# Kernel optimization log

Hardware: AMD Instinct MI355X
Metric: run time of the kernel (lower is better)

Reference implementation:

```python
import jax, jax.numpy as jnp
import numpy as np

B, T, C = 4, 1024, 512      # batch, seq_len, n_attn
H, TT, D = 1, 1024, 16      # n_head (forced to 1 by kv.view), ctx_len, head_size


def setup_inputs() -> dict:
    key = jax.random.key(0)
    ks = jax.random.split(key, 13)
    s = 0.02
    return {
        "x": jax.random.normal(ks[0], (B, T, C), jnp.float32),
        "time_w": 1.0 + 0.1 * jax.random.normal(ks[1], (H, TT), jnp.float32),
        "time_alpha": 1.0 + 0.1 * jax.random.normal(ks[2], (H, 1, TT), jnp.float32),
        "time_beta": 1.0 + 0.1 * jax.random.normal(ks[3], (H, TT, 1), jnp.float32),
        "time_gamma": 1.0 + 0.1 * jax.random.normal(ks[4], (TT, 1), jnp.float32),
        "Wk": s * jax.random.normal(ks[5], (D, C), jnp.float32),
        "bk": jnp.zeros((D,), jnp.float32),
        "Wv": s * jax.random.normal(ks[6], (D, C), jnp.float32),
        "bv": jnp.zeros((D,), jnp.float32),
        "Wr": s * jax.random.normal(ks[7], (D, C), jnp.float32),
        "br": jnp.zeros((D,), jnp.float32),
        "Wo": s * jax.random.normal(ks[8], (64, D), jnp.float32),
        "bo": jnp.zeros((64,), jnp.float32),
    }


def reference(x, time_w, time_alpha, time_beta, time_gamma,
              Wk, bk, Wv, bv, Wr, br, Wo, bo):
    Tq = x.shape[1]
    # --- Toeplitz decay-matrix build (pad / tile / reshape trick) ---
    w = jnp.pad(time_w, ((0, 0), (0, TT)))                    # [H, 2TT]
    w = jnp.tile(w, (1, TT))[:, :-TT]                         # [H, 2TT*TT - TT]
    w = w.reshape(-1, TT, 2 * TT - 1)[:, :, TT - 1:]          # [H, TT, TT]
    w = w[:, :Tq, :Tq] * time_alpha[:, :, :Tq] * time_beta[:, :Tq, :]  # [H, T, T]
    # --- time shift on first half of channels (ZeroPad2d((0,0,1,-1))) ---
    half = x.shape[-1] // 2
    xs = jnp.pad(x[:, :, :half], ((0, 0), (1, 0), (0, 0)))[:, :-1]   # shift right by 1
    xx = jnp.concatenate([xs, x[:, :, half:]], axis=-1)              # [B, T, C]
    # --- k / v / r projections ---
    k = jnp.exp(jnp.clip(xx @ Wk.T + bk, -60.0, 30.0))        # [B, T, D]
    v = xx @ Wv.T + bv                                        # [B, T, D]
    r = xx @ Wr.T + br                                        # [B, T, D]
    sum_k = jnp.cumsum(k, axis=1)                             # [B, T, D]
    kv = k * v                                                # [B, T, D]
    # torch: kv.view(B,T,1,D).transpose(1,2) -> [B,1,T,D]; einsum 'htu,bthd->bhud'
    # broadcasts w's h=1 against kv's time axis and kv's t=1 against w's t axis:
    #   wkv[b,h,u,d] = (sum_t w[0,t,u]) * kv[b,h(time),d]
    w_sum = jnp.sum(w, axis=1)[0]                             # [T] over u
    wkv_full = w_sum[None, None, :, None] * kv[:, :, None, :] # [B, T, T, D]
    wkv = jnp.mean(wkv_full, axis=1)                          # mean over h -> [B, T, D]
    rwkv = r * wkv / (sum_k + 1e-8)                           # [B, T, D]
    out = (rwkv @ Wo.T + bo) * time_gamma[:Tq, :]             # [B, T, 64]
    return out
```

## Files before the change

kernel.cpp:

```cpp
#include <hip/hip_runtime.h>
#include <hip/hip_bf16.h>

typedef __hip_bfloat16 bf16;


__device__ __forceinline__ float ldf(const void* p, int f, long idx) {
    if (f == 0) return ((const float*)p)[idx];
    if (f == 1) {
        unsigned int u = ((unsigned int)((const unsigned short*)p)[idx]) << 16;
        float r; __builtin_memcpy(&r, &u, 4); return r;
    }
    return 0.f;
}

__device__ __forceinline__ int sniff_one(const unsigned short* u, int els) {
    int n16 = els < 64 ? els : 64;
    bool allzero = true;
    for (int j = 0; j < n16; ++j) if (u[j] != 0) { allzero = false; break; }
    if (allzero) return 2;
    int npair = n16 / 2;
    for (int j = 0; j < npair; ++j) {
        unsigned short lo = u[2 * j], hi = u[2 * j + 1];
        int elo = (lo >> 7) & 0xFF, ehi = (hi >> 7) & 0xFF;
        bool lo_ok = (elo >= 64 && elo <= 190) || lo == 0;
        bool hi_ok = (ehi >= 64 && ehi <= 190) || hi == 0;
        if (!(lo_ok && hi_ok)) return 0;
    }
    return 1;
}

__global__ __launch_bounds__(256) void setup_kernel(
    const void* x, const void* tw, const void* alpha, const void* beta,
    const void* gamma, const void* Wk, const void* bk, const void* Wv,
    const void* bv, const void* Wr, const void* br, const void* Wo,
    const void* bo,
    int n0, int n1, int n2, int n3, int n4, int n5, int n6, int n7,
    int n8, int n9, int n10, int n11, int n12,
    int* __restrict__ flags,
    float* __restrict__ WT4, float* __restrict__ biasWS,
    float* __restrict__ WoF, float* __restrict__ boF,
    float* __restrict__ gammaF, float* __restrict__ w_sum)
{
    __shared__ int sf[16];
    __shared__ float red[256];
    int tid = threadIdx.x;
    const void* ps[13] = {x,tw,alpha,beta,gamma,Wk,bk,Wv,bv,Wr,br,Wo,bo};
    int ns[13] = {n0,n1,n2,n3,n4,n5,n6,n7,n8,n9,n10,n11,n12};
    if (tid < 13) sf[tid] = sniff_one((const unsigned short*)ps[tid], ns[tid]);
    __syncthreads();
    if (tid == 0) {
        int any16 = 0;
        for (int j = 0; j < 13; ++j) if (sf[j] == 1) any16 = 1;
        sf[13] = any16;
    }
    __syncthreads();
    if (blockIdx.x == 0 && tid < 14) flags[tid] = sf[tid];

    int idx = blockIdx.x * 256 + tid;
    if (idx < 32768) {
        int q = idx >> 8, rem = idx & 255;
        int o = rem >> 2, c = q * 4 + (rem & 3);
        float val = 0.f;
        if (o < 16)      val = ldf(Wk, sf[5], (long)o * 512 + c);
        else if (o < 32) val = ldf(Wv, sf[7], (long)(o - 16) * 512 + c);
        else if (o < 48) val = ldf(Wr, sf[9], (long)(o - 32) * 512 + c);
        WT4[idx] = val;
    } else if (idx < 33792) {
        int i = idx - 32768;
        WoF[i] = ldf(Wo, sf[11], i);
    } else if (idx < 34816) {
        int i = idx - 33792;
        gammaF[i] = ldf(gamma, sf[4], i);
    } else if (idx < 34880) {
        int i = idx - 34816;
        boF[i] = ldf(bo, sf[12], i);
    } else if (idx < 34944) {
        int i = idx - 34880;
        float bb = 0.f;
        if (i < 16)      bb = ldf(bk, sf[6], i);
        else if (i < 32) bb = ldf(bv, sf[8], i - 16);
        else if (i < 48) bb = ldf(br, sf[10], i - 32);
        biasWS[i] = bb;
    }

    int u = blockIdx.x;
    int ftw = sf[1], fal = sf[2], fbe = sf[3];
    float acc = 0.f;
    int n = 1024 - u;
    for (int s = tid; s < n; s += 256)
        acc += ldf(tw, ftw, 1023 - s) * ldf(beta, fbe, u + s);
    red[tid] = acc;
    __syncthreads();
    for (int off = 128; off > 0; off >>= 1) {
        if (tid < off) red[tid] += red[tid + off];
        __syncthreads();
    }
    if (tid == 0) w_sum[u] = red[0] * ldf(alpha, fal, u);
}

__global__ __launch_bounds__(256) void proj_kernel(
    const void* __restrict__ x, const float* __restrict__ WT4,
    const float* __restrict__ biasWS, const int* __restrict__ flg,
    float* __restrict__ k_ws, float* __restrict__ v_ws, float* __restrict__ r_ws)
{
    __shared__ float xs[8 * 512];
    __shared__ float red[16 * 8 * 64];
    int tid = threadIdx.x;
    int row0 = blockIdx.x * 8;
    int b = row0 >> 10;
    int lt0 = row0 & 1023;
    int fx = flg[0];

    if (fx == 1) {
        const unsigned short* xp = (const unsigned short*)x;
        #pragma unroll
        for (int j = 0; j < 4; ++j) {
            int v = tid + 256 * j;
            int el = v * 4;
            int r = el >> 9, c = el & 511;
            int lt = lt0 + r - ((c < 256) ? 1 : 0);
            float4 f;
            if (lt < 0) f = make_float4(0.f, 0.f, 0.f, 0.f);
            else {
                const unsigned short* sp = xp + ((long)(b * 1024 + lt) * 512 + c);
                unsigned int u0 = ((unsigned int)sp[0]) << 16;
                unsigned int u1 = ((unsigned int)sp[1]) << 16;
                unsigned int u2 = ((unsigned int)sp[2]) << 16;
                unsigned int u3 = ((unsigned int)sp[3]) << 16;
                __builtin_memcpy(&f.x, &u0, 4); __builtin_memcpy(&f.y, &u1, 4);
                __builtin_memcpy(&f.z, &u2, 4); __builtin_memcpy(&f.w, &u3, 4);
            }
            reinterpret_cast<float4*>(xs)[v] = f;
        }
    } else {
        const float* xp = (const float*)x;
        #pragma unroll
        for (int j = 0; j < 4; ++j) {
            int v = tid + 256 * j;
            int el = v * 4;
            int r = el >> 9, c = el & 511;
            int lt = lt0 + r - ((c < 256) ? 1 : 0);
            float4 f;
            if (lt < 0) f = make_float4(0.f, 0.f, 0.f, 0.f);
            else f = *reinterpret_cast<const float4*>(xp + ((long)(b * 1024 + lt) * 512 + c));
            reinterpret_cast<float4*>(xs)[v] = f;
        }
    }
    __syncthreads();

    int o4 = tid & 15, cc = tid >> 4;
    const float4* xs4 = reinterpret_cast<const float4*>(xs);
    const float4* W4 = reinterpret_cast<const float4*>(WT4);
    float a0[8], a1[8], a2[8], a3[8];
    #pragma unroll
    for (int r = 0; r < 8; ++r) { a0[r] = a1[r] = a2[r] = a3[r] = 0.f; }
    #pragma unroll
    for (int q = 0; q < 8; ++q) {
        int cq = cc * 8 + q;
        float4 w0 = W4[cq * 64 + o4 * 4 + 0];
        float4 w1 = W4[cq * 64 + o4 * 4 + 1];
        float4 w2 = W4[cq * 64 + o4 * 4 + 2];
        float4 w3 = W4[cq * 64 + o4 * 4 + 3];
        #pragma unroll
        for (int r = 0; r < 8; ++r) {
            float4 x4 = xs4[r * 128 + cq];
            a0[r] += x4.x * w0.x + x4.y * w0.y + x4.z * w0.z + x4.w * w0.w;
            a1[r] += x4.x * w1.x + x4.y * w1.y + x4.z * w1.z + x4.w * w1.w;
            a2[r] += x4.x * w2.x + x4.y * w2.y + x4.z * w2.z + x4.w * w2.w;
            a3[r] += x4.x * w3.x + x4.y * w3.y + x4.z * w3.z + x4.w * w3.w;
        }
    }
    float4* red4 = reinterpret_cast<float4*>(red);
    #pragma unroll
    for (int r = 0; r < 8; ++r)
        red4[(cc * 8 + r) * 16 + o4] = make_float4(a0[r], a1[r], a2[r], a3[r]);
    __syncthreads();

    #pragma unroll
    for (int it = 0; it < 2; ++it) {
        int idx = tid + 256 * it;
        int o2 = idx & 63, r2 = idx >> 6;
        float s = biasWS[o2];
        #pragma unroll
        for (int cc2 = 0; cc2 < 16; ++cc2)
            s += red[(cc2 * 8 + r2) * 64 + o2];
        if (o2 < 48) {
            int d = o2 & 15;
            long a = (long)(lt0 + r2) * 64 + b * 16 + d;
            if (o2 < 16)      k_ws[a] = expf(fminf(fmaxf(s, -60.f), 30.f));
            else if (o2 < 32) v_ws[a] = s;
            else              r_ws[a] = s;
        }
    }
}

__global__ __launch_bounds__(64) void scanA_kernel(
    const float* __restrict__ k_ws, const float* __restrict__ v_ws,
    float* __restrict__ segsum, float* __restrict__ segkv)
{
    int seg = blockIdx.x, bd = threadIdx.x;
    float part = 0.f, kvp = 0.f;
    for (int i = 0; i < 64; ++i) {
        long a = (long)(seg * 64 + i) * 64 + bd;
        float kk = k_ws[a];
        part += kk;
        kvp += kk * v_ws[a];
    }
    segsum[seg * 64 + bd] = part;
    segkv[seg * 64 + bd] = kvp;
}

__global__ __launch_bounds__(64) void scanB_kernel(
    float* k_ws, const float* __restrict__ segsum,
    const float* __restrict__ segkv, float* __restrict__ kvmean)
{
    int seg = blockIdx.x, bd = threadIdx.x;
    float run = 0.f;
    for (int s = 0; s < seg; ++s) run += segsum[s * 64 + bd];
    for (int i = 0; i < 64; ++i) {
        long a = (long)(seg * 64 + i) * 64 + bd;
        run += k_ws[a];
        k_ws[a] = run;
    }
    if (seg == 0) {
        float kvt = 0.f;
        for (int s = 0; s < 16; ++s) kvt += segkv[s * 64 + bd];
        kvmean[bd] = kvt * (1.0f / 1024.0f);
    }
}

__global__ __launch_bounds__(256) void out_kernel(
    const float* __restrict__ r_ws, const float* __restrict__ cumk,
    const float* __restrict__ kvmean, const float* __restrict__ w_sum,
    const float* __restrict__ WoF, const float* __restrict__ boF,
    const float* __restrict__ gammaF, const int* __restrict__ flg,
    void* __restrict__ out)
{
    int tid = threadIdx.x;
    int rl = tid >> 6, o = tid & 63;
    int row = blockIdx.x * 4 + rl;
    int b = row >> 10, t = row & 1023;
    __shared__ float rw[4][16];
    if (o < 16) {
        long a = (long)t * 64 + b * 16 + o;
        rw[rl][o] = r_ws[a] * w_sum[t] * kvmean[b * 16 + o] / (cumk[a] + 1e-8f);
    }
    __syncthreads();
    float acc = boF[o];
    const float4* W4 = reinterpret_cast<const float4*>(WoF + o * 16);
    #pragma unroll
    for (int j = 0; j < 4; ++j) {
        float4 w = W4[j];
        acc += rw[rl][4 * j + 0] * w.x + rw[rl][4 * j + 1] * w.y +
               rw[rl][4 * j + 2] * w.z + rw[rl][4 * j + 3] * w.w;
    }
    float val = acc * gammaF[t];
    if (flg[13]) ((bf16*)out)[(long)row * 64 + o] = __float2bfloat16(val);
    else         ((float*)out)[(long)row * 64 + o] = val;
}

extern "C" void kernel_launch(void* const* d_in, const int* in_sizes, int n_in,
                              void* d_out, int out_size, void* d_ws, size_t ws_size,
                              hipStream_t stream) {
    const void* x     = d_in[0];
    const void* tw    = d_in[1];
    const void* alpha = d_in[2];
    const void* beta  = d_in[3];
    const void* gamma = d_in[4];
    const void* Wk    = d_in[5];
    const void* bk    = d_in[6];
    const void* Wv    = d_in[7];
    const void* bv    = d_in[8];
    const void* Wr    = d_in[9];
    const void* br    = d_in[10];
    const void* Wo    = d_in[11];
    const void* bo    = d_in[12];

    float* ws     = (float*)d_ws;
    float* k_ws   = ws;
    float* v_ws   = ws + 65536;
    float* r_ws   = ws + 131072;
    float* WT4    = ws + 196608;
    float* biasWS = ws + 229376;
    float* WoF    = ws + 229440;
    float* boF    = ws + 230464;
    float* gammaF = ws + 230528;
    float* kvmean = ws + 231552;
    float* w_sum  = ws + 231616;
    float* segsum = ws + 232640;
    float* segkv  = ws + 233664;
    int*   flags  = (int*)(ws + 234688);

    setup_kernel<<<1024, 256, 0, stream>>>(
        x, tw, alpha, beta, gamma, Wk, bk, Wv, bv, Wr, br, Wo, bo,
        in_sizes[0], in_sizes[1], in_sizes[2], in_sizes[3], in_sizes[4],
        in_sizes[5], in_sizes[6], in_sizes[7], in_sizes[8], in_sizes[9],
        in_sizes[10], in_sizes[11], in_sizes[12],
        flags, WT4, biasWS, WoF, boF, gammaF, w_sum);
    proj_kernel<<<512, 256, 0, stream>>>(x, WT4, biasWS, flags,
                                         k_ws, v_ws, r_ws);
    scanA_kernel<<<16, 64, 0, stream>>>(k_ws, v_ws, segsum, segkv);
    scanB_kernel<<<16, 64, 0, stream>>>(k_ws, segsum, segkv, kvmean);
    out_kernel<<<1024, 256, 0, stream>>>(r_ws, k_ws, kvmean, w_sum,
                                         WoF, boF, gammaF, flags, (void*)d_out);
}
```

Baseline: 114.3 us.

## Fuse segment reductions into projection via atomics and move w_sum into scan kernel

The segment-sum and k·v partial reductions from the first scan kernel now happen inside the projection epilogue through atomicAdd into zeroed segment buffers. The v workspace and one kernel launch go away. The Toeplitz w_sum reduction moves from the 1024-block setup kernel into extra threads of the scan kernel, so setup shrinks to 145 blocks. The cost is atomic contention, recomputing exp(k) in the v lanes, and a serial 1024-step per-thread loop for w_sum on only 16 blocks.

```diff
diff --git a/kernel.cpp b/kernel.cpp
--- a/kernel.cpp
+++ b/kernel.cpp
@@ -39,22 +39,23 @@
     int* __restrict__ flags,
     float* __restrict__ WT4, float* __restrict__ biasWS,
     float* __restrict__ WoF, float* __restrict__ boF,
-    float* __restrict__ gammaF, float* __restrict__ w_sum)
+    float* __restrict__ gammaF, float* __restrict__ segzero)
 {
     __shared__ int sf[16];
-    __shared__ float red[256];
     int tid = threadIdx.x;
     const void* ps[13] = {x,tw,alpha,beta,gamma,Wk,bk,Wv,bv,Wr,br,Wo,bo};
     int ns[13] = {n0,n1,n2,n3,n4,n5,n6,n7,n8,n9,n10,n11,n12};
     if (tid < 13) sf[tid] = sniff_one((const unsigned short*)ps[tid], ns[tid]);
     __syncthreads();
-    if (tid == 0) {
-        int any16 = 0;
-        for (int j = 0; j < 13; ++j) if (sf[j] == 1) any16 = 1;
-        sf[13] = any16;
-    }
-    __syncthreads();
-    if (blockIdx.x == 0 && tid < 14) flags[tid] = sf[tid];
+    if (blockIdx.x == 0 && tid < 14) {
+        if (tid == 13) {
+            int any16 = 0;
+            for (int j = 0; j < 13; ++j) if (sf[j] == 1) any16 = 1;
+            flags[13] = any16;
+        } else {
+            flags[tid] = sf[tid];
+        }
+    }
 
     int idx = blockIdx.x * 256 + tid;
     if (idx < 32768) {
@@ -81,27 +82,16 @@
         else if (i < 32) bb = ldf(bv, sf[8], i - 16);
         else if (i < 48) bb = ldf(br, sf[10], i - 32);
         biasWS[i] = bb;
-    }
-
-    int u = blockIdx.x;
-    int ftw = sf[1], fal = sf[2], fbe = sf[3];
-    float acc = 0.f;
-    int n = 1024 - u;
-    for (int s = tid; s < n; s += 256)
-        acc += ldf(tw, ftw, 1023 - s) * ldf(beta, fbe, u + s);
-    red[tid] = acc;
-    __syncthreads();
-    for (int off = 128; off > 0; off >>= 1) {
-        if (tid < off) red[tid] += red[tid + off];
-        __syncthreads();
-    }
-    if (tid == 0) w_sum[u] = red[0] * ldf(alpha, fal, u);
+    } else if (idx < 36992) {
+        segzero[idx - 34944] = 0.f;
+    }
 }
 
 __global__ __launch_bounds__(256) void proj_kernel(
     const void* __restrict__ x, const float* __restrict__ WT4,
     const float* __restrict__ biasWS, const int* __restrict__ flg,
-    float* __restrict__ k_ws, float* __restrict__ v_ws, float* __restrict__ r_ws)
+    float* __restrict__ k_ws, float* __restrict__ r_ws,
+    float* __restrict__ segsum, float* __restrict__ segkv)
 {
     __shared__ float xs[8 * 512];
     __shared__ float red[16 * 8 * 64];
@@ -176,6 +166,7 @@
         red4[(cc * 8 + r) * 16 + o4] = make_float4(a0[r], a1[r], a2[r], a3[r]);
     __syncthreads();
 
+    int seg = lt0 >> 6;
     #pragma unroll
     for (int it = 0; it < 2; ++it) {
         int idx = tid + 256 * it;
@@ -184,48 +175,54 @@
         #pragma unroll
         for (int cc2 = 0; cc2 < 16; ++cc2)
             s += red[(cc2 * 8 + r2) * 64 + o2];
-        if (o2 < 48) {
-            int d = o2 & 15;
-            long a = (long)(lt0 + r2) * 64 + b * 16 + d;
-            if (o2 < 16)      k_ws[a] = expf(fminf(fmaxf(s, -60.f), 30.f));
-            else if (o2 < 32) v_ws[a] = s;
-            else              r_ws[a] = s;
-        }
-    }
-}
-
-__global__ __launch_bounds__(64) void scanA_kernel(
-    const float* __restrict__ k_ws, const float* __restrict__ v_ws,
-    float* __restrict__ segsum, float* __restrict__ segkv)
+        long a = (long)(lt0 + r2) * 64 + b * 16 + (o2 & 15);
+        if (o2 < 16) {
+            k_ws[a] = expf(fminf(fmaxf(s, -60.f), 30.f));
+        } else if (o2 < 32) {
+            int d = o2 - 16;
+            float sk = biasWS[d];
+            #pragma unroll
+            for (int cc2 = 0; cc2 < 16; ++cc2)
+                sk += red[(cc2 * 8 + r2) * 64 + d];
+            float kk = expf(fminf(fmaxf(sk, -60.f), 30.f));
+            atomicAdd(&segsum[seg * 64 + b * 16 + d], kk);
+            atomicAdd(&segkv[seg * 64 + b * 16 + d], kk * s);
+        } else if (o2 < 48) {
+            r_ws[a] = s;
+        }
+    }
+}
+
+__global__ __launch_bounds__(128) void scanB_kernel(
+    float* k_ws, const float* __restrict__ segsum,
+    const float* __restrict__ segkv, float* __restrict__ kvmean,
+    const void* __restrict__ tw, const void* __restrict__ alpha,
+    const void* __restrict__ beta, const int* __restrict__ flg,
+    float* __restrict__ w_sum)
 {
-    int seg = blockIdx.x, bd = threadIdx.x;
-    float part = 0.f, kvp = 0.f;
-    for (int i = 0; i < 64; ++i) {
-        long a = (long)(seg * 64 + i) * 64 + bd;
-        float kk = k_ws[a];
-        part += kk;
-        kvp += kk * v_ws[a];
-    }
-    segsum[seg * 64 + bd] = part;
-    segkv[seg * 64 + bd] = kvp;
-}
-
-__global__ __launch_bounds__(64) void scanB_kernel(
-    float* k_ws, const float* __restrict__ segsum,
-    const float* __restrict__ segkv, float* __restrict__ kvmean)
-{
-    int seg = blockIdx.x, bd = threadIdx.x;
-    float run = 0.f;
-    for (int s = 0; s < seg; ++s) run += segsum[s * 64 + bd];
-    for (int i = 0; i < 64; ++i) {
-        long a = (long)(seg * 64 + i) * 64 + bd;
-        run += k_ws[a];
-        k_ws[a] = run;
-    }
-    if (seg == 0) {
-        float kvt = 0.f;
-        for (int s = 0; s < 16; ++s) kvt += segkv[s * 64 + bd];
-        kvmean[bd] = kvt * (1.0f / 1024.0f);
+    int seg = blockIdx.x, tid = threadIdx.x;
+    if (tid < 64) {
+        int bd = tid;
+        float run = 0.f;
+        for (int s = 0; s < seg; ++s) run += segsum[s * 64 + bd];
+        for (int i = 0; i < 64; ++i) {
+            long a = (long)(seg * 64 + i) * 64 + bd;
+            run += k_ws[a];
+            k_ws[a] = run;
+        }
+        if (seg == 0) {
+            float kvt = 0.f;
+            for (int s = 0; s < 16; ++s) kvt += segkv[s * 64 + bd];
+            kvmean[bd] = kvt * (1.0f / 1024.0f);
+        }
+    } else {
+        int u = seg * 64 + (tid - 64);
+        int ftw = flg[1], fal = flg[2], fbe = flg[3];
+        float acc = 0.f;
+        int n = 1024 - u;
+        for (int s = 0; s < n; ++s)
+            acc += ldf(tw, ftw, 1023 - s) * ldf(beta, fbe, u + s);
+        w_sum[u] = acc * ldf(alpha, fal, u);
     }
 }
 
@@ -278,29 +275,28 @@
 
     float* ws     = (float*)d_ws;
     float* k_ws   = ws;
-    float* v_ws   = ws + 65536;
-    float* r_ws   = ws + 131072;
-    float* WT4    = ws + 196608;
-    float* biasWS = ws + 229376;
-    float* WoF    = ws + 229440;
-    float* boF    = ws + 230464;
-    float* gammaF = ws + 230528;
-    float* kvmean = ws + 231552;
-    float* w_sum  = ws + 231616;
-    float* segsum = ws + 232640;
-    float* segkv  = ws + 233664;
-    int*   flags  = (int*)(ws + 234688);
-
-    setup_kernel<<<1024, 256, 0, stream>>>(
+    float* r_ws   = ws + 65536;
+    float* WT4    = ws + 131072;
+    float* biasWS = ws + 163840;
+    float* WoF    = ws + 163904;
+    float* boF    = ws + 164928;
+    float* gammaF = ws + 164992;
+    float* kvmean = ws + 166016;
+    float* w_sum  = ws + 166080;
+    float* segsum = ws + 167104;
+    float* segkv  = ws + 168128;
+    int*   flags  = (int*)(ws + 169152);
+
+    setup_kernel<<<145, 256, 0, stream>>>(
         x, tw, alpha, beta, gamma, Wk, bk, Wv, bv, Wr, br, Wo, bo,
         in_sizes[0], in_sizes[1], in_sizes[2], in_sizes[3], in_sizes[4],
         in_sizes[5], in_sizes[6], in_sizes[7], in_sizes[8], in_sizes[9],
         in_sizes[10], in_sizes[11], in_sizes[12],
-        flags, WT4, biasWS, WoF, boF, gammaF, w_sum);
+        flags, WT4, biasWS, WoF, boF, gammaF, segsum );
     proj_kernel<<<512, 256, 0, stream>>>(x, WT4, biasWS, flags,
-                                         k_ws, v_ws, r_ws);
-    scanA_kernel<<<16, 64, 0, stream>>>(k_ws, v_ws, segsum, segkv);
-    scanB_kernel<<<16, 64, 0, stream>>>(k_ws, segsum, segkv, kvmean);
+                                         k_ws, r_ws, segsum, segkv);
+    scanB_kernel<<<16, 128, 0, stream>>>(k_ws, segsum, segkv, kvmean,
+                                         tw, alpha, beta, flags, w_sum);
     out_kernel<<<1024, 256, 0, stream>>>(r_ws, k_ws, kvmean, w_sum,
                                          WoF, boF, gammaF, flags, (void*)d_out);
 }
```

New measurement: 246.2 us. 115% more time.
